# Performance work log

Measured on AMD Instinct MI355X. Metric: run time of the kernel, lower is better.

The kernel has to match this reference:

```python
import jax, jax.numpy as jnp
import numpy as np

N = 4096  # out_features (rows of W)
M = 4096  # in_features (cols of W)
S = 2048  # number of Givens pairs per side (= N//2)
TOKENS = 2048
EPS = 1e-8


def setup_inputs() -> dict:
    key = jax.random.key(0)
    ks = jax.random.split(key, 6)
    x = jax.random.normal(ks[0], (TOKENS, M), dtype=jnp.float32)
    W = jax.random.normal(ks[1], (N, M), dtype=jnp.float32) * (1.0 / np.sqrt(M))
    bias = jax.random.normal(ks[2], (N,), dtype=jnp.float32) * 0.02
    theta_L = 0.02 * jax.random.normal(ks[3], (S,), dtype=jnp.float32)
    theta_R = 0.02 * jax.random.normal(ks[4], (S,), dtype=jnp.float32)
    ecd_log_mag = jnp.zeros((N,), dtype=jnp.float32)
    # disjoint index pairs: (0,1),(2,3),... as produced by a permutation reshape
    pairs_L = jnp.arange(N, dtype=jnp.int64).reshape(S, 2)
    pairs_R = jnp.arange(M, dtype=jnp.int64).reshape(S, 2)
    return {"x": x, "W": W, "bias": bias, "theta_L": theta_L,
            "theta_R": theta_R, "ecd_log_mag": ecd_log_mag,
            "pairs_L": pairs_L, "pairs_R": pairs_R}


def _apply_left_rotations(W, theta, pairs):
    # Plane (Givens) rotations on disjoint row pairs of W: [S] angles, [S,2] indices
    c = jnp.cos(theta)[:, None]
    s = jnp.sin(theta)[:, None]
    i, j = pairs[:, 0], pairs[:, 1]
    ri, rj = W[i], W[j]                       # [S, M] gathers
    return W.at[i].set(c * ri - s * rj).at[j].set(s * ri + c * rj)


def _apply_right_rotations(W, theta, pairs):
    # Plane rotations on disjoint column pairs of W
    c = jnp.cos(theta)
    s = jnp.sin(theta)
    p, q = pairs[:, 0], pairs[:, 1]
    cp, cq = W[:, p], W[:, q]                 # [N, S] gathers
    return W.at[:, p].set(c * cp - s * cq).at[:, q].set(s * cp + c * cq)


def reference(x, W, bias, theta_L, theta_R, ecd_log_mag, pairs_L, pairs_R):
    # base row norms are buffers computed under no_grad from the frozen base weight
    base_row_norms = jax.lax.stop_gradient(jnp.linalg.norm(W, axis=1))  # [N]
    Wp = _apply_left_rotations(W, theta_L, pairs_L)
    Wp = _apply_right_rotations(Wp, theta_R, pairs_R)
    # magnitude rescale: row-normalize rotated weight, scale by learned magnitude
    row_norm = jnp.linalg.norm(Wp, axis=1, keepdims=True)               # [N,1]
    mag = base_row_norms * jnp.exp(ecd_log_mag)                         # [N]
    W_eff = Wp * (mag[:, None] / (row_norm + EPS))                      # [N,M]
    return x @ W_eff.T + bias                                           # [T,N]
```

## Files before the change

kernel.cpp:

```cpp
#include <hip/hip_runtime.h>
#include <hip/hip_bf16.h>


#define GK 4096
#define GN 4096
#define GT 2048
#define NPAIR 2048

typedef __bf16 bf16x8 __attribute__((ext_vector_type(8)));
typedef float  f32x4  __attribute__((ext_vector_type(4)));

static __device__ __forceinline__ unsigned short f2bf(float f) {
    union { float f; unsigned int u; } v; v.f = f;
    unsigned int r = v.u + 0x7fffu + ((v.u >> 16) & 1u);
    return (unsigned short)(r >> 16);
}
static __device__ __forceinline__ unsigned int pack2bf(float a, float b) {
    return (unsigned int)f2bf(a) | ((unsigned int)f2bf(b) << 16);
}

__global__ __launch_bounds__(256) void sincos_pre(
    const float* __restrict__ thR, float2* __restrict__ csR)
{
    const int i = blockIdx.x * 256 + threadIdx.x;
    if (i < NPAIR) {
        const float t = thR[i];
        csR[i] = make_float2(cosf(t), sinf(t));
    }
}

__global__ __launch_bounds__(256) void prelude(
    const float* __restrict__ W, const float* __restrict__ thL,
    const float2* __restrict__ csR, const float* __restrict__ ecd,
    const float* __restrict__ x,
    unsigned short* __restrict__ Weff, unsigned short* __restrict__ Xbf)
{
    const int tid = threadIdx.x;

    if (blockIdx.x >= 2048) {
        const int cb = blockIdx.x - 2048;
        const size_t base = (size_t)cb * 512;
        const float4* X4 = (const float4*)x;
        uint4* O4 = (uint4*)Xbf;
#pragma unroll
        for (int k = 0; k < 2; k++) {
            const size_t m = base + tid + k * 256;
            const float4 a = X4[2 * m];
            const float4 b = X4[2 * m + 1];
            uint4 o;
            o.x = pack2bf(a.x, a.y);
            o.y = pack2bf(a.z, a.w);
            o.z = pack2bf(b.x, b.y);
            o.w = pack2bf(b.z, b.w);
            O4[m] = o;
        }
        return;
    }

    const int s  = blockIdx.x;
    const int i0 = 2 * s, i1 = 2 * s + 1;

    const float tl = thL[s];
    const float cL = cosf(tl), sL = sinf(tl);

    float4 b0[4], b1[4];
    float s00 = 0.f, s11 = 0.f, s01 = 0.f;

    const float4* r0  = (const float4*)(W + (size_t)i0 * GK);
    const float4* r1  = (const float4*)(W + (size_t)i1 * GK);
    const float4* CS4 = (const float4*)csR;

#pragma unroll
    for (int k = 0; k < 4; k++) {
        const int c4 = tid + k * 256;
        const float4 w0 = r0[c4];
        const float4 w1 = r1[c4];
        const float4 cs = CS4[c4];
        s00 += w0.x * w0.x + w0.y * w0.y + w0.z * w0.z + w0.w * w0.w;
        s11 += w1.x * w1.x + w1.y * w1.y + w1.z * w1.z + w1.w * w1.w;
        s01 += w0.x * w1.x + w0.y * w1.y + w0.z * w1.z + w0.w * w1.w;
        const float a0x = cL * w0.x - sL * w1.x;
        const float a0y = cL * w0.y - sL * w1.y;
        const float a0z = cL * w0.z - sL * w1.z;
        const float a0w = cL * w0.w - sL * w1.w;
        const float a1x = sL * w0.x + cL * w1.x;
        const float a1y = sL * w0.y + cL * w1.y;
        const float a1z = sL * w0.z + cL * w1.z;
        const float a1w = sL * w0.w + cL * w1.w;
        b0[k].x = cs.x * a0x - cs.y * a0y;
        b0[k].y = cs.y * a0x + cs.x * a0y;
        b0[k].z = cs.z * a0z - cs.w * a0w;
        b0[k].w = cs.w * a0z + cs.z * a0w;
        b1[k].x = cs.x * a1x - cs.y * a1y;
        b1[k].y = cs.y * a1x + cs.x * a1y;
        b1[k].z = cs.z * a1z - cs.w * a1w;
        b1[k].w = cs.w * a1z + cs.z * a1w;
    }

#pragma unroll
    for (int off = 32; off; off >>= 1) {
        s00 += __shfl_down(s00, off);
        s11 += __shfl_down(s11, off);
        s01 += __shfl_down(s01, off);
    }
    __shared__ float red[3][4];
    __shared__ float scales[2];
    const int wave = tid >> 6, lane = tid & 63;
    if (lane == 0) { red[0][wave] = s00; red[1][wave] = s11; red[2][wave] = s01; }
    __syncthreads();
    if (tid == 0) {
        const float t0 = red[0][0] + red[0][1] + red[0][2] + red[0][3];
        const float t1 = red[1][0] + red[1][1] + red[1][2] + red[1][3];
        const float td = red[2][0] + red[2][1] + red[2][2] + red[2][3];
        const float n0 = cL * cL * t0 + sL * sL * t1 - 2.f * cL * sL * td;
        const float n1 = sL * sL * t0 + cL * cL * t1 + 2.f * cL * sL * td;
        scales[0] = sqrtf(t0) * expf(ecd[i0]) / (sqrtf(n0) + 1e-8f);
        scales[1] = sqrtf(t1) * expf(ecd[i1]) / (sqrtf(n1) + 1e-8f);
    }
    __syncthreads();
    const float sc0 = scales[0], sc1 = scales[1];

    uint2* o0 = (uint2*)(Weff + (size_t)i0 * GK);
    uint2* o1 = (uint2*)(Weff + (size_t)i1 * GK);
#pragma unroll
    for (int k = 0; k < 4; k++) {
        const int c4 = tid + k * 256;
        uint2 p0, p1;
        p0.x = pack2bf(b0[k].x * sc0, b0[k].y * sc0);
        p0.y = pack2bf(b0[k].z * sc0, b0[k].w * sc0);
        p1.x = pack2bf(b1[k].x * sc1, b1[k].y * sc1);
        p1.y = pack2bf(b1[k].z * sc1, b1[k].w * sc1);
        o0[c4] = p0;
        o1[c4] = p1;
    }
}

static __device__ __forceinline__ void glds16(const unsigned short* g, unsigned short* l) {
    __builtin_amdgcn_global_load_lds(
        (const __attribute__((address_space(1))) unsigned int*)g,
        (__attribute__((address_space(3))) unsigned int*)l, 16, 0, 0);
}

__global__ __launch_bounds__(256) void gemm_bt(
    const unsigned short* __restrict__ A,
    const unsigned short* __restrict__ B,
    const float* __restrict__ bias,
    float* __restrict__ C)
{
    constexpr int BM = 128, BN = 128, BK = 32;
    __shared__ unsigned short As[BM * BK];
    __shared__ unsigned short Bs[BN * BK];

    const int tid  = threadIdx.x;
    const int lane = tid & 63;
    const int wave = tid >> 6;
    const int quad = lane >> 4;
    const int l16  = lane & 15;
    const int wm   = wave >> 1;
    const int wn   = wave & 1;
    const int bm   = blockIdx.y * BM;
    const int bn   = blockIdx.x * BN;

    const int srow = wave * 32 + (lane >> 2);
    const int scol = (lane & 3) * 8;
    const unsigned short* gA0 = A + (size_t)(bm + srow) * GK + scol;
    const unsigned short* gA1 = A + (size_t)(bm + srow + 16) * GK + scol;
    const unsigned short* gB0 = B + (size_t)(bn + srow) * GK + scol;
    const unsigned short* gB1 = B + (size_t)(bn + srow + 16) * GK + scol;
    unsigned short* lA0 = &As[srow * BK + scol];
    unsigned short* lA1 = &As[(srow + 16) * BK + scol];
    unsigned short* lB0 = &Bs[srow * BK + scol];
    unsigned short* lB1 = &Bs[(srow + 16) * BK + scol];

    f32x4 acc[4][4] = {};

    for (int k0 = 0; k0 < GK; k0 += BK) {
        __syncthreads();
        glds16(gA0 + k0, lA0);
        glds16(gA1 + k0, lA1);
        glds16(gB0 + k0, lB0);
        glds16(gB1 + k0, lB1);
        __syncthreads();

        bf16x8 aF[4], bF[4];
#pragma unroll
        for (int i = 0; i < 4; i++)
            aF[i] = *(const bf16x8*)&As[(wm * 64 + i * 16 + l16) * BK + quad * 8];
#pragma unroll
        for (int j = 0; j < 4; j++)
            bF[j] = *(const bf16x8*)&Bs[(wn * 64 + j * 16 + l16) * BK + quad * 8];
#pragma unroll
        for (int i = 0; i < 4; i++)
#pragma unroll
            for (int j = 0; j < 4; j++)
                acc[i][j] = __builtin_amdgcn_mfma_f32_16x16x32_bf16(
                    aF[i], bF[j], acc[i][j], 0, 0, 0);
    }

#pragma unroll
    for (int i = 0; i < 4; i++) {
        const int m = bm + wm * 64 + i * 16 + quad * 4;
#pragma unroll
        for (int j = 0; j < 4; j++) {
            const int n = bn + wn * 64 + j * 16 + l16;
            const float bv = bias[n];
#pragma unroll
            for (int r = 0; r < 4; r++)
                C[(size_t)(m + r) * GN + n] = acc[i][j][r] + bv;
        }
    }
}

extern "C" void kernel_launch(void* const* d_in, const int* in_sizes, int n_in,
                              void* d_out, int out_size, void* d_ws, size_t ws_size,
                              hipStream_t stream) {
    const float* x    = (const float*)d_in[0];
    const float* W    = (const float*)d_in[1];
    const float* bias = (const float*)d_in[2];
    const float* thL  = (const float*)d_in[3];
    const float* thR  = (const float*)d_in[4];
    const float* ecd  = (const float*)d_in[5];

    unsigned short* Weff = (unsigned short*)d_ws;
    unsigned short* Xbf  = (unsigned short*)((char*)d_ws + (size_t)GN * GK * 2);
    float2* csR = (float2*)((char*)d_ws + (size_t)GN * GK * 2 + (size_t)GT * GK * 2);

    float* out = (float*)d_out;

    sincos_pre<<<dim3(NPAIR / 256), dim3(256), 0, stream>>>(thR, csR);
    prelude<<<dim3(4096), dim3(256), 0, stream>>>(W, thL, csR, ecd, x, Weff, Xbf);
    gemm_bt<<<dim3(GN / 128, GT / 128), dim3(256), 0, stream>>>(Xbf, Weff, bias, out);
}
```

Measured before the change: 227.8 us.

## Double-buffer GEMM LDS tiles with BK=64 and XOR-swizzled layout

Rewrites the GEMM main loop to use two LDS buffers with BK=64. The next tile is issued via global_load_lds before computing the current one, with an explicit vmcnt wait and barriers, so global loads overlap the MFMA work. An XOR swizzle on the 16-byte chunks is meant to cut LDS bank conflicts on fragment reads, and launch bounds now request 2 blocks per CU. In exchange, LDS use grows to 64KB per block, which may limit occupancy, and the hand-written waitcnt/barrier sequencing is fragile.

```diff
diff --git a/kernel.cpp b/kernel.cpp
--- a/kernel.cpp
+++ b/kernel.cpp
@@ -141,15 +141,15 @@
         (__attribute__((address_space(3))) unsigned int*)l, 16, 0, 0);
 }
 
-__global__ __launch_bounds__(256) void gemm_bt(
+__global__ __launch_bounds__(256, 2) void gemm_bt(
     const unsigned short* __restrict__ A,
     const unsigned short* __restrict__ B,
     const float* __restrict__ bias,
     float* __restrict__ C)
 {
-    constexpr int BM = 128, BN = 128, BK = 32;
-    __shared__ unsigned short As[BM * BK];
-    __shared__ unsigned short Bs[BN * BK];
+    constexpr int BM = 128, BN = 128, BK = 64;
+    constexpr int NT = GK / BK;
+    __shared__ unsigned short smem[2][2][BM * BK];
 
     const int tid  = threadIdx.x;
     const int lane = tid & 63;
@@ -161,41 +161,71 @@
     const int bm   = blockIdx.y * BM;
     const int bn   = blockIdx.x * BN;
 
-    const int srow = wave * 32 + (lane >> 2);
-    const int scol = (lane & 3) * 8;
-    const unsigned short* gA0 = A + (size_t)(bm + srow) * GK + scol;
-    const unsigned short* gA1 = A + (size_t)(bm + srow + 16) * GK + scol;
-    const unsigned short* gB0 = B + (size_t)(bn + srow) * GK + scol;
-    const unsigned short* gB1 = B + (size_t)(bn + srow + 16) * GK + scol;
-    unsigned short* lA0 = &As[srow * BK + scol];
-    unsigned short* lA1 = &As[(srow + 16) * BK + scol];
-    unsigned short* lB0 = &Bs[srow * BK + scol];
-    unsigned short* lB1 = &Bs[(srow + 16) * BK + scol];
+    const int lrow = lane >> 3;
+    const int jlog = (lane & 7) ^ lrow;
+    const unsigned short* gA[4];
+    const unsigned short* gB[4];
+    int loff[4];
+#pragma unroll
+    for (int j = 0; j < 4; j++) {
+        const int chunk = j * 4 + wave;
+        gA[j] = A + (size_t)(bm + chunk * 8 + lrow) * GK + jlog * 8;
+        gB[j] = B + (size_t)(bn + chunk * 8 + lrow) * GK + jlog * 8;
+        loff[j] = chunk * 512 + lane * 8;
+    }
+
+#define STAGE(buf, k0) do {                                               \
+    _Pragma("unroll")                                                     \
+    for (int j = 0; j < 4; j++) {                                         \
+        glds16(gA[j] + (k0), &smem[buf][0][loff[j]]);                     \
+        glds16(gB[j] + (k0), &smem[buf][1][loff[j]]);                     \
+    } } while (0)
 
     f32x4 acc[4][4] = {};
 
-    for (int k0 = 0; k0 < GK; k0 += BK) {
-        __syncthreads();
-        glds16(gA0 + k0, lA0);
-        glds16(gA1 + k0, lA1);
-        glds16(gB0 + k0, lB0);
-        glds16(gB1 + k0, lB1);
-        __syncthreads();
-
-        bf16x8 aF[4], bF[4];
-#pragma unroll
-        for (int i = 0; i < 4; i++)
-            aF[i] = *(const bf16x8*)&As[(wm * 64 + i * 16 + l16) * BK + quad * 8];
-#pragma unroll
-        for (int j = 0; j < 4; j++)
-            bF[j] = *(const bf16x8*)&Bs[(wn * 64 + j * 16 + l16) * BK + quad * 8];
-#pragma unroll
-        for (int i = 0; i < 4; i++)
-#pragma unroll
-            for (int j = 0; j < 4; j++)
-                acc[i][j] = __builtin_amdgcn_mfma_f32_16x16x32_bf16(
-                    aF[i], bF[j], acc[i][j], 0, 0, 0);
-    }
+#define COMPUTE(b) do {                                                   \
+    const unsigned short* As_ = &smem[b][0][0];                           \
+    const unsigned short* Bs_ = &smem[b][1][0];                           \
+    bf16x8 aF[2][4], bF[2][4];                                            \
+    _Pragma("unroll")                                                     \
+    for (int kk = 0; kk < 2; kk++) {                                      \
+        _Pragma("unroll")                                                 \
+        for (int i = 0; i < 4; i++) {                                     \
+            const int ps = ((quad + 4 * kk) ^ (l16 & 7)) * 8;             \
+            aF[kk][i] = *(const bf16x8*)(As_ + (wm * 64 + i * 16 + l16) * BK + ps); \
+            bF[kk][i] = *(const bf16x8*)(Bs_ + (wn * 64 + i * 16 + l16) * BK + ps); \
+        } }                                                               \
+    _Pragma("unroll")                                                     \
+    for (int i = 0; i < 4; i++) {                                         \
+        _Pragma("unroll")                                                 \
+        for (int j = 0; j < 4; j++) {                                     \
+            acc[i][j] = __builtin_amdgcn_mfma_f32_16x16x32_bf16(          \
+                aF[0][i], bF[0][j], acc[i][j], 0, 0, 0);                  \
+            acc[i][j] = __builtin_amdgcn_mfma_f32_16x16x32_bf16(          \
+                aF[1][i], bF[1][j], acc[i][j], 0, 0, 0);                  \
+        } }                                                               \
+    } while (0)
+
+    STAGE(0, 0);
+    int cur = 0;
+    for (int t = 0; t < NT - 1; ++t) {
+        STAGE(cur ^ 1, (t + 1) * BK);
+        __builtin_amdgcn_sched_barrier(0);
+        asm volatile("s_waitcnt vmcnt(8)" ::: "memory");
+        __builtin_amdgcn_s_barrier();
+        __builtin_amdgcn_sched_barrier(0);
+        COMPUTE(cur);
+        __builtin_amdgcn_sched_barrier(0);
+        __builtin_amdgcn_s_barrier();
+        cur ^= 1;
+    }
+    asm volatile("s_waitcnt vmcnt(0)" ::: "memory");
+    __builtin_amdgcn_s_barrier();
+    __builtin_amdgcn_sched_barrier(0);
+    COMPUTE(cur);
+
+#undef STAGE
+#undef COMPUTE
 
 #pragma unroll
     for (int i = 0; i < 4; i++) {
```

New measurement: 210.6 us. 1.08x faster.
